# Performance work log

Measured on AMD Instinct MI355X. Metric: run time of the kernel, lower is better.

## Reference

```python
import jax, jax.numpy as jnp
import numpy as np


def setup_inputs() -> dict:
    key = jax.random.key(0)
    k1, k2, k3, k4 = jax.random.split(key, 4)
    B, T, D = 32, 2048, 128
    queries = jax.random.normal(k1, (B, T, D), dtype=jnp.float32)
    keys = jax.random.normal(k2, (B, T, D), dtype=jnp.float32)
    values = jax.random.normal(k3, (B, T, D), dtype=jnp.float32)
    valid_lens = jax.random.randint(k4, (B,), 0, T, dtype=jnp.int32)
    return {"queries": queries, "keys": keys, "values": values, "valid_lens": valid_lens}


def reference(queries, keys, values, valid_lens):
    d = queries.shape[-1]
    scale = d / 0.5  # faithful to source: 2*d, NOT sqrt(d)
    # (B, Tq, Tk) scores
    scores = jnp.einsum('bqd,bkd->bqk', queries, keys) / scale
    T = scores.shape[-1]
    # lengths (B,) -> mask (B, 1, Tk), broadcast over query rows
    mask = jnp.arange(T) < valid_lens[:, None, None]
    neg_inf = jnp.finfo(scores.dtype).min
    logits = jnp.where(mask, scores, neg_inf)
    probs = jax.nn.softmax(logits, axis=-1)
    fully_masked = ~jnp.any(mask, axis=-1, keepdims=True)
    probs = jnp.where(fully_masked, jnp.zeros_like(probs), probs)
    # dropout p=0.0 -> identity
    return jnp.einsum('bqk,bkv->bqv', probs, values)
```

## Files before the change

### kernel.cpp

```cpp
#include <hip/hip_runtime.h>
#include <hip/hip_bf16.h>

#define B_ 32
#define T_ 2048
#define D_ 128
#define BQ 64
#define BK 64

typedef __attribute__((ext_vector_type(8))) __bf16 bf16x8;
typedef __attribute__((ext_vector_type(16))) float f32x16;

__device__ __forceinline__ float fast_exp2(float x) {
#if __has_builtin(__builtin_amdgcn_exp2f)
    return __builtin_amdgcn_exp2f(x);
#else
    return exp2f(x);
#endif
}

__device__ __forceinline__ f32x16 zero16() {
    f32x16 z;
    #pragma unroll
    for (int i = 0; i < 16; ++i) z[i] = 0.f;
    return z;
}

__global__ __launch_bounds__(256, 4)
void prep_k(const float* __restrict__ K, const int* __restrict__ vlens,
            __hip_bfloat16* __restrict__ Kb)
{
    const int b = blockIdx.y, k0 = blockIdx.x * 64;
    const int kmax = (vlens[b] + 63) & ~63;
    if (k0 >= kmax) return;
    const float4* src = (const float4*)(K + ((size_t)b * T_ + k0) * D_);
    uint2* dst = (uint2*)(Kb + ((size_t)b * T_ + k0) * D_);
    #pragma unroll
    for (int it = 0; it < 8; ++it) {
        int c = it * 256 + threadIdx.x;
        float4 v = src[c];
        union { __hip_bfloat16 h[4]; uint2 u; } pk;
        pk.h[0] = __float2bfloat16(v.x); pk.h[1] = __float2bfloat16(v.y);
        pk.h[2] = __float2bfloat16(v.z); pk.h[3] = __float2bfloat16(v.w);
        dst[c] = pk.u;
    }
}

__global__ __launch_bounds__(256, 2)
void prep_vt(const float* __restrict__ V, const int* __restrict__ vlens,
             __hip_bfloat16* __restrict__ VTb)
{
    __shared__ float tile[64][132];
    const int b = blockIdx.y, k0 = blockIdx.x * 64;
    const int kmax = (vlens[b] + 63) & ~63;
    if (k0 >= kmax) return;
    const float4* src = (const float4*)(V + ((size_t)b * T_ + k0) * D_);
    #pragma unroll
    for (int it = 0; it < 8; ++it) {
        int c = it * 256 + threadIdx.x;
        int row = c >> 5, c4 = c & 31;
        *(float4*)&tile[row][c4 * 4] = src[c];
    }
    __syncthreads();
    #pragma unroll
    for (int it = 0; it < 8; ++it) {
        int c = it * 256 + threadIdx.x;
        int kc = c & 15, d = c >> 4;
        union { __hip_bfloat16 h[4]; uint2 u; } pk;
        #pragma unroll
        for (int j = 0; j < 4; ++j) {
            int jj = (j + kc) & 3;
            pk.h[jj] = __float2bfloat16(tile[kc * 4 + jj][d]);
        }
        *(uint2*)(VTb + ((size_t)b * D_ + d) * T_ + k0 + kc * 4) = pk.u;
    }
}

__global__ __launch_bounds__(128, 2)
void attn_main(const float* __restrict__ Q, const int* __restrict__ vlens,
               const __hip_bfloat16* __restrict__ Kb,
               const __hip_bfloat16* __restrict__ VTb,
               float* __restrict__ out)
{
    const int tid  = threadIdx.x;
    const int wave = tid >> 6;
    const int lane = tid & 63;
    const int l32  = lane & 31;
    const int hi   = lane >> 5;

    const int b    = blockIdx.y;
    const int q0   = blockIdx.x * BQ;
    const int vlen = vlens[b];
    const int nkb  = (vlen + 63) >> 6;

    __shared__ __hip_bfloat16 sK [64][136];
    __shared__ __hip_bfloat16 sVT[128][72];
    __shared__ __hip_bfloat16 sP [64][72];

    bf16x8 qf[8];
    {
        const float* qp = Q + ((size_t)b * T_ + q0 + wave * 32 + l32) * D_ + hi * 8;
        #pragma unroll
        for (int ds = 0; ds < 8; ++ds) {
            const float4* p4 = (const float4*)(qp + ds * 16);
            float4 a = p4[0], c = p4[1];
            __hip_bfloat16 h[8] = {
                __float2bfloat16(a.x), __float2bfloat16(a.y),
                __float2bfloat16(a.z), __float2bfloat16(a.w),
                __float2bfloat16(c.x), __float2bfloat16(c.y),
                __float2bfloat16(c.z), __float2bfloat16(c.w) };
            qf[ds] = *(const bf16x8*)h;
        }
    }

    bf16x8 ones;
    #pragma unroll
    for (int j = 0; j < 8; ++j) ones[j] = (__bf16)1.0f;

    f32x16 o[4];
    #pragma unroll
    for (int dt = 0; dt < 4; ++dt) o[dt] = zero16();
    f32x16 lacc = zero16();

    const float C = 1.4426950408889634f / 256.0f;

    for (int kb = 0; kb < nkb; ++kb) {
        const int k0 = kb * 64;
        __syncthreads();

        {
            const __hip_bfloat16* kbase = Kb + ((size_t)b * T_ + k0) * D_;
            #pragma unroll
            for (int it = 0; it < 8; ++it) {
                int c = it * 128 + tid;
                int row = c >> 4, cc = c & 15;
                uint4 v = *(const uint4*)(kbase + row * D_ + cc * 8);
                *(uint4*)&sK[row][cc * 8] = v;
            }
            const __hip_bfloat16* vbase = VTb + (size_t)b * D_ * T_ + k0;
            #pragma unroll
            for (int it = 0; it < 8; ++it) {
                int c = it * 128 + tid;
                int d = c >> 3, cc = c & 7;
                uint4 v = *(const uint4*)(vbase + (size_t)d * T_ + cc * 8);
                *(uint4*)&sVT[d][cc * 8] = v;
            }
        }
        __syncthreads();

        f32x16 s[2];
        s[0] = zero16(); s[1] = zero16();
        #pragma unroll
        for (int nt = 0; nt < 2; ++nt)
            #pragma unroll
            for (int ds = 0; ds < 8; ++ds) {
                bf16x8 kf = *(const bf16x8*)&sK[nt * 32 + l32][ds * 16 + hi * 8];
                s[nt] = __builtin_amdgcn_mfma_f32_32x32x16_bf16(qf[ds], kf, s[nt], 0, 0, 0);
            }

        #pragma unroll
        for (int nt = 0; nt < 2; ++nt) {
            const bool valid = (k0 + nt * 32 + l32) < vlen;
            #pragma unroll
            for (int r = 0; r < 16; ++r) {
                float e = fast_exp2(s[nt][r] * C);
                e = valid ? e : 0.f;
                int q = (r & 3) + 8 * (r >> 2) + 4 * hi + wave * 32;
                sP[q][nt * 32 + l32] = __float2bfloat16(e);
            }
        }

        #pragma unroll
        for (int ks = 0; ks < 4; ++ks) {
            bf16x8 pf = *(const bf16x8*)&sP[wave * 32 + l32][ks * 16 + hi * 8];
            lacc = __builtin_amdgcn_mfma_f32_32x32x16_bf16(pf, ones, lacc, 0, 0, 0);
            #pragma unroll
            for (int dt = 0; dt < 4; ++dt) {
                bf16x8 vf = *(const bf16x8*)&sVT[dt * 32 + l32][ks * 16 + hi * 8];
                o[dt] = __builtin_amdgcn_mfma_f32_32x32x16_bf16(pf, vf, o[dt], 0, 0, 0);
            }
        }
    }

    float inv[16];
    #pragma unroll
    for (int r = 0; r < 16; ++r) inv[r] = (lacc[r] > 0.f) ? 1.0f / lacc[r] : 0.f;
    #pragma unroll
    for (int dt = 0; dt < 4; ++dt)
        #pragma unroll
        for (int r = 0; r < 16; ++r) {
            int q = (r & 3) + 8 * (r >> 2) + 4 * hi + wave * 32;
            out[((size_t)b * T_ + q0 + q) * D_ + dt * 32 + l32] = o[dt][r] * inv[r];
        }
}

extern "C" void kernel_launch(void* const* d_in, const int* in_sizes, int n_in,
                              void* d_out, int out_size, void* d_ws, size_t ws_size,
                              hipStream_t stream) {
    const float* Q = (const float*)d_in[0];
    const float* K = (const float*)d_in[1];
    const float* V = (const float*)d_in[2];
    const int* vl  = (const int*)d_in[3];
    float* out     = (float*)d_out;

    const size_t kb_bytes = (size_t)B_ * T_ * D_ * 2;
    if (ws_size < 2 * kb_bytes) return;
    __hip_bfloat16* Kb  = (__hip_bfloat16*)d_ws;
    __hip_bfloat16* VTb = (__hip_bfloat16*)((char*)d_ws + kb_bytes);

    prep_k <<<dim3(T_ / 64, B_), 256, 0, stream>>>(K, vl, Kb);
    prep_vt<<<dim3(T_ / 64, B_), 256, 0, stream>>>(V, vl, VTb);
    attn_main<<<dim3(T_ / BQ, B_), 128, 0, stream>>>(Q, vl, Kb, VTb, out);
}
```

Before: 235.2 us.

## Double-buffer K/V tiles, keep P in registers via permlane swap, widen query block

Computes S transposed so the softmax probabilities can be repacked into MFMA A-operand fragments in registers with v_permlane32_swap, which removes the shared-memory P round trip. The row-sum MFMA against a ones vector is replaced with scalar accumulation plus a shuffle. K/V tiles are double-buffered in LDS with register prefetch of the next tile, and the block grows to 4 waves covering 128 queries so each loaded K/V tile is reused by more queries. It adds s_setprio hints around the MFMA sections, in exchange for higher register and LDS pressure and fewer blocks in flight.

```diff
diff --git a/kernel.cpp b/kernel.cpp
--- a/kernel.cpp
+++ b/kernel.cpp
@@ -1,10 +1,11 @@
 #include <hip/hip_runtime.h>
 #include <hip/hip_bf16.h>
+#include <stdint.h>
 
 #define B_ 32
 #define T_ 2048
 #define D_ 128
-#define BQ 64
+#define BQ 128
 #define BK 64
 
 typedef __attribute__((ext_vector_type(8))) __bf16 bf16x8;
@@ -23,6 +24,16 @@
     #pragma unroll
     for (int i = 0; i < 16; ++i) z[i] = 0.f;
     return z;
+}
+
+__device__ __forceinline__ uint32_t pk2(float a, float b) {
+    union { __hip_bfloat16 h; unsigned short u; } ua, ub;
+    ua.h = __float2bfloat16(a); ub.h = __float2bfloat16(b);
+    return (uint32_t)ua.u | ((uint32_t)ub.u << 16);
+}
+
+__device__ __forceinline__ void plswap(uint32_t& a, uint32_t& b) {
+    asm("v_permlane32_swap_b32 %0, %1" : "+v"(a), "+v"(b));
 }
 
 __global__ __launch_bounds__(256, 4)
@@ -75,7 +86,7 @@
     }
 }
 
-__global__ __launch_bounds__(128, 2)
+__global__ __launch_bounds__(256, 2)
 void attn_main(const float* __restrict__ Q, const int* __restrict__ vlens,
                const __hip_bfloat16* __restrict__ Kb,
                const __hip_bfloat16* __restrict__ VTb,
@@ -92,9 +103,8 @@
     const int vlen = vlens[b];
     const int nkb  = (vlen + 63) >> 6;
 
-    __shared__ __hip_bfloat16 sK [64][136];
-    __shared__ __hip_bfloat16 sVT[128][72];
-    __shared__ __hip_bfloat16 sP [64][72];
+    __shared__ __hip_bfloat16 sK [2][64][136];
+    __shared__ __hip_bfloat16 sVT[2][128][72];
 
     bf16x8 qf[8];
     {
@@ -112,84 +122,125 @@
         }
     }
 
-    bf16x8 ones;
-    #pragma unroll
-    for (int j = 0; j < 8; ++j) ones[j] = (__bf16)1.0f;
-
     f32x16 o[4];
     #pragma unroll
     for (int dt = 0; dt < 4; ++dt) o[dt] = zero16();
-    f32x16 lacc = zero16();
+    float lsum = 0.f;
 
     const float C = 1.4426950408889634f / 256.0f;
 
+    const __hip_bfloat16* kb_base = Kb  + (size_t)b * T_ * D_;
+    const __hip_bfloat16* vt_base = VTb + (size_t)b * D_ * T_;
+
+    uint4 kreg[4], vreg[4];
+
+    if (nkb > 0) {
+        #pragma unroll
+        for (int it = 0; it < 4; ++it) {
+            int c = it * 256 + tid;
+            kreg[it] = *(const uint4*)(kb_base + (size_t)(c >> 4) * D_ + (c & 15) * 8);
+            vreg[it] = *(const uint4*)(vt_base + (size_t)(c >> 3) * T_ + (c & 7) * 8);
+        }
+        #pragma unroll
+        for (int it = 0; it < 4; ++it) {
+            int c = it * 256 + tid;
+            *(uint4*)&sK [0][c >> 4][(c & 15) * 8] = kreg[it];
+            *(uint4*)&sVT[0][c >> 3][(c & 7)  * 8] = vreg[it];
+        }
+    }
+    __syncthreads();
+
+    int cur = 0;
     for (int kb = 0; kb < nkb; ++kb) {
         const int k0 = kb * 64;
-        __syncthreads();
-
-        {
-            const __hip_bfloat16* kbase = Kb + ((size_t)b * T_ + k0) * D_;
-            #pragma unroll
-            for (int it = 0; it < 8; ++it) {
-                int c = it * 128 + tid;
-                int row = c >> 4, cc = c & 15;
-                uint4 v = *(const uint4*)(kbase + row * D_ + cc * 8);
-                *(uint4*)&sK[row][cc * 8] = v;
-            }
-            const __hip_bfloat16* vbase = VTb + (size_t)b * D_ * T_ + k0;
-            #pragma unroll
-            for (int it = 0; it < 8; ++it) {
-                int c = it * 128 + tid;
-                int d = c >> 3, cc = c & 7;
-                uint4 v = *(const uint4*)(vbase + (size_t)d * T_ + cc * 8);
-                *(uint4*)&sVT[d][cc * 8] = v;
-            }
-        }
-        __syncthreads();
+        const bool pfetch = (kb + 1 < nkb);
+
+        if (pfetch) {
+            const __hip_bfloat16* kp = kb_base + (size_t)(k0 + 64) * D_;
+            const __hip_bfloat16* vp = vt_base + (k0 + 64);
+            #pragma unroll
+            for (int it = 0; it < 4; ++it) {
+                int c = it * 256 + tid;
+                kreg[it] = *(const uint4*)(kp + (size_t)(c >> 4) * D_ + (c & 15) * 8);
+                vreg[it] = *(const uint4*)(vp + (size_t)(c >> 3) * T_ + (c & 7) * 8);
+            }
+        }
 
         f32x16 s[2];
         s[0] = zero16(); s[1] = zero16();
-        #pragma unroll
-        for (int nt = 0; nt < 2; ++nt)
-            #pragma unroll
-            for (int ds = 0; ds < 8; ++ds) {
-                bf16x8 kf = *(const bf16x8*)&sK[nt * 32 + l32][ds * 16 + hi * 8];
-                s[nt] = __builtin_amdgcn_mfma_f32_32x32x16_bf16(qf[ds], kf, s[nt], 0, 0, 0);
-            }
-
+        __builtin_amdgcn_s_setprio(1);
+        #pragma unroll
+        for (int ds = 0; ds < 8; ++ds) {
+            bf16x8 kf0 = *(const bf16x8*)&sK[cur][l32     ][ds * 16 + hi * 8];
+            bf16x8 kf1 = *(const bf16x8*)&sK[cur][32 + l32][ds * 16 + hi * 8];
+            s[0] = __builtin_amdgcn_mfma_f32_32x32x16_bf16(kf0, qf[ds], s[0], 0, 0, 0);
+            s[1] = __builtin_amdgcn_mfma_f32_32x32x16_bf16(kf1, qf[ds], s[1], 0, 0, 0);
+        }
+        __builtin_amdgcn_s_setprio(0);
+
+        bf16x8 pf[4];
         #pragma unroll
         for (int nt = 0; nt < 2; ++nt) {
-            const bool valid = (k0 + nt * 32 + l32) < vlen;
+            const int kbase_l = k0 + nt * 32 + 4 * hi;
+            float p[16];
             #pragma unroll
             for (int r = 0; r < 16; ++r) {
+                int krow = (r & 3) + 8 * (r >> 2);
                 float e = fast_exp2(s[nt][r] * C);
-                e = valid ? e : 0.f;
-                int q = (r & 3) + 8 * (r >> 2) + 4 * hi + wave * 32;
-                sP[q][nt * 32 + l32] = __float2bfloat16(e);
-            }
-        }
-
-        #pragma unroll
-        for (int ks = 0; ks < 4; ++ks) {
-            bf16x8 pf = *(const bf16x8*)&sP[wave * 32 + l32][ks * 16 + hi * 8];
-            lacc = __builtin_amdgcn_mfma_f32_32x32x16_bf16(pf, ones, lacc, 0, 0, 0);
+                p[r] = (kbase_l + krow < vlen) ? e : 0.f;
+            }
+            lsum += (((p[0] + p[1]) + (p[2] + p[3])) + ((p[4] + p[5]) + (p[6] + p[7])))
+                  + (((p[8] + p[9]) + (p[10] + p[11])) + ((p[12] + p[13]) + (p[14] + p[15])));
+            #pragma unroll
+            for (int k2 = 0; k2 < 2; ++k2) {
+                const int base = k2 * 8;
+                uint32_t A0 = pk2(p[base + 0], p[base + 1]);
+                uint32_t B0 = pk2(p[base + 4], p[base + 5]);
+                uint32_t A1 = pk2(p[base + 2], p[base + 3]);
+                uint32_t B1 = pk2(p[base + 6], p[base + 7]);
+                plswap(A0, B0);
+                plswap(A1, B1);
+                union { uint32_t u[4]; bf16x8 v; } fr;
+                fr.u[0] = A0; fr.u[1] = A1; fr.u[2] = B0; fr.u[3] = B1;
+                pf[nt * 2 + k2] = fr.v;
+            }
+        }
+
+        __builtin_amdgcn_s_setprio(1);
+        #pragma unroll
+        for (int ks = 0; ks < 4; ++ks)
             #pragma unroll
             for (int dt = 0; dt < 4; ++dt) {
-                bf16x8 vf = *(const bf16x8*)&sVT[dt * 32 + l32][ks * 16 + hi * 8];
-                o[dt] = __builtin_amdgcn_mfma_f32_32x32x16_bf16(pf, vf, o[dt], 0, 0, 0);
-            }
-        }
-    }
-
-    float inv[16];
-    #pragma unroll
-    for (int r = 0; r < 16; ++r) inv[r] = (lacc[r] > 0.f) ? 1.0f / lacc[r] : 0.f;
+                bf16x8 vf = *(const bf16x8*)&sVT[cur][dt * 32 + l32][ks * 16 + hi * 8];
+                o[dt] = __builtin_amdgcn_mfma_f32_32x32x16_bf16(pf[ks], vf, o[dt], 0, 0, 0);
+            }
+        __builtin_amdgcn_s_setprio(0);
+
+        if (pfetch) {
+            const int nxt = cur ^ 1;
+            #pragma unroll
+            for (int it = 0; it < 4; ++it) {
+                int c = it * 256 + tid;
+                *(uint4*)&sK [nxt][c >> 4][(c & 15) * 8] = kreg[it];
+                *(uint4*)&sVT[nxt][c >> 3][(c & 7)  * 8] = vreg[it];
+            }
+        }
+        __syncthreads();
+        cur ^= 1;
+    }
+
+    lsum += __shfl_xor(lsum, 32);
+    float inv = (lsum > 0.f) ? 1.0f / lsum : 0.f;
+    float invr[16];
+    #pragma unroll
+    for (int r = 0; r < 16; ++r)
+        invr[r] = __shfl(inv, (r & 3) + 8 * (r >> 2) + 4 * hi);
     #pragma unroll
     for (int dt = 0; dt < 4; ++dt)
         #pragma unroll
         for (int r = 0; r < 16; ++r) {
-            int q = (r & 3) + 8 * (r >> 2) + 4 * hi + wave * 32;
-            out[((size_t)b * T_ + q0 + q) * D_ + dt * 32 + l32] = o[dt][r] * inv[r];
+            int q = (r & 3) + 8 * (r >> 2) + 4 * hi;
+            out[((size_t)b * T_ + q0 + wave * 32 + q) * D_ + dt * 32 + l32] = o[dt][r] * invr[r];
         }
 }
 
@@ -209,5 +260,5 @@
 
     prep_k <<<dim3(T_ / 64, B_), 256, 0, stream>>>(K, vl, Kb);
     prep_vt<<<dim3(T_ / 64, B_), 256, 0, stream>>>(V, vl, VTb);
-    attn_main<<<dim3(T_ / BQ, B_), 128, 0, stream>>>(Q, vl, Kb, VTb, out);
-}
+    attn_main<<<dim3(T_ / BQ, B_), 256, 0, stream>>>(Q, vl, Kb, VTb, out);
+}
```

Result: slower. 286.8 us (+21.9%).
